# Performance work log

Hardware: AMD Instinct MI355X
Metric: run time of the kernel (lower is better)

## Reference

```python
import jax, jax.numpy as jnp
import numpy as np

K = 2  # top-k experts per token


def setup_inputs() -> dict:
    key = jax.random.key(0)
    k1, k2, k3, k4 = jax.random.split(key, 4)
    B, S, D, E = 4, 4096, 1024, 64
    x = jax.random.normal(k1, (B, S, D), dtype=jnp.float32)
    gate_w = jax.random.normal(k2, (E, D), dtype=jnp.float32) * (1.0 / np.sqrt(D))
    noise_weight = jax.random.normal(k3, (E,), dtype=jnp.float32) * 0.02
    noise = jax.random.normal(k4, (B, S, E), dtype=jnp.float32)  # randn_like(logits) * noisy_std(=1.0)
    return {"x": x, "gate_w": gate_w, "noise_weight": noise_weight, "noise": noise}


def reference(x, gate_w, noise_weight, noise):
    E = gate_w.shape[0]
    # logits = x @ W^T  -> [B, S, E]
    logits = jnp.einsum("bsd,ed->bse", x, gate_w)
    logits_noisy = logits + noise * noise_weight  # noisy_std = 1.0 folded into `noise`
    top_vals, top_idx = jax.lax.top_k(logits_noisy, K)  # [B,S,K]
    # scatter top-k logits into a -inf mask, then softmax over experts
    keep = jax.nn.one_hot(top_idx, E, dtype=jnp.bool_).any(axis=-2)  # [B,S,E]
    neg_inf = jnp.finfo(logits_noisy.dtype).min
    sparse = jnp.where(keep, logits_noisy, neg_inf)
    weights = jax.nn.softmax(sparse, axis=-1)
    return weights, top_idx
```

## Files before the change

### kernel.cpp

```cpp
#include <hip/hip_runtime.h>
#include <math.h>


#define DDIM 1024
#define NEXP 64
#define NTOK 16384

typedef float f4 __attribute__((ext_vector_type(4)));
typedef short s8 __attribute__((ext_vector_type(8)));
typedef unsigned int u32;

static __device__ __forceinline__ void split3(float f, short& h, short& m, short& l) {
    const u32 uf = __float_as_uint(f);
    h = (short)(uf >> 16);
    const float r1 = f - __uint_as_float(uf & 0xffff0000u);
    const u32 u1 = __float_as_uint(r1);
    m = (short)(u1 >> 16);
    const float r2 = r1 - __uint_as_float(u1 & 0xffff0000u);
    l = (short)(__float_as_uint(r2) >> 16);
}

__global__ __launch_bounds__(256)
void w_prep(const float* __restrict__ gw, short* __restrict__ wimg) {
    const int uid = blockIdx.x * 256 + threadIdx.x;
    const int c   = uid >> 9;
    const int kk  = (uid >> 8) & 1;
    const int e   = (uid >> 2) & 63;
    const int q   = uid & 3;
    const int k0  = c * 64 + kk * 32 + q * 8;
    const float* src = gw + (size_t)e * DDIM + k0;
    s8 hv, mv, lv;
    #pragma unroll
    for (int j = 0; j < 8; ++j) {
        short h, m, l;
        split3(src[j], h, m, l);
        hv[j] = h; mv[j] = m; lv[j] = l;
    }
    const size_t base = (size_t)c * 1536 + (kk * 3) * 256
                      + (e >> 4) * 64 + q * 16 + (e & 15);
    *(s8*)(wimg + (base      ) * 8) = hv;
    *(s8*)(wimg + (base + 256) * 8) = mv;
    *(s8*)(wimg + (base + 512) * 8) = lv;
}

__global__ __launch_bounds__(256, 4)
void gate_fused(const float* __restrict__ x,
                const short* __restrict__ wimg,
                const float* __restrict__ noise_weight,
                const float* __restrict__ noise,
                float* __restrict__ out_w,
                float* __restrict__ out_i)
{
    __shared__ float L[16][66];

    const int tid  = threadIdx.x;
    const int lane = tid & 63;
    const int wv   = tid >> 6;
    const int m    = lane & 15;
    const int q    = lane >> 4;
    const int tokBase = blockIdx.x * 16;

    const float* xrow = x + (size_t)(tokBase + m) * DDIM + q * 8;
    const short* wb   = wimg + ((size_t)wv * 64 + lane) * 8;

    const float nw = noise_weight[lane];
    float nz[4];
    #pragma unroll
    for (int tt = 0; tt < 4; ++tt)
        nz[tt] = noise[(size_t)(tokBase + wv * 4 + tt) * NEXP + lane];

    f4 acc0 = (f4)0.f, acc1 = (f4)0.f;

    f4 sa[2][4];
    s8 b[2][6];

    sa[0][0] = *(const f4*)(xrow);
    sa[0][1] = *(const f4*)(xrow + 4);
    sa[0][2] = *(const f4*)(xrow + 32);
    sa[0][3] = *(const f4*)(xrow + 36);
    #pragma unroll
    for (int i = 0; i < 6; ++i)
        b[0][i] = *(const s8*)(wb + (size_t)i * (256 * 8));

    #pragma unroll 2
    for (int cc = 0; cc < 16; ++cc) {
        const int cur = cc & 1;
        const int nxt = cur ^ 1;

        if (cc + 1 < 16) {
            const float* s = xrow + (cc + 1) * 64;
            sa[nxt][0] = *(const f4*)(s);
            sa[nxt][1] = *(const f4*)(s + 4);
            sa[nxt][2] = *(const f4*)(s + 32);
            sa[nxt][3] = *(const f4*)(s + 36);
            const short* p = wb + (size_t)(cc + 1) * (1536 * 8);
            #pragma unroll
            for (int i = 0; i < 6; ++i)
                b[nxt][i] = *(const s8*)(p + (size_t)i * (256 * 8));
        }

        s8 ah[2], am_[2], al[2];
        const float* sv = (const float*)sa[cur];
        #pragma unroll
        for (int kk = 0; kk < 2; ++kk)
            #pragma unroll
            for (int j = 0; j < 8; ++j) {
                short h, mm, l;
                split3(sv[kk * 8 + j], h, mm, l);
                ah[kk][j] = h; am_[kk][j] = mm; al[kk][j] = l;
            }

        acc0 = __builtin_amdgcn_mfma_f32_16x16x32_bf16(ah[0], b[cur][0], acc0, 0, 0, 0);
        acc1 = __builtin_amdgcn_mfma_f32_16x16x32_bf16(ah[0], b[cur][1], acc1, 0, 0, 0);
        acc1 = __builtin_amdgcn_mfma_f32_16x16x32_bf16(am_[0], b[cur][0], acc1, 0, 0, 0);
        acc1 = __builtin_amdgcn_mfma_f32_16x16x32_bf16(ah[0], b[cur][2], acc1, 0, 0, 0);
        acc1 = __builtin_amdgcn_mfma_f32_16x16x32_bf16(am_[0], b[cur][1], acc1, 0, 0, 0);
        acc1 = __builtin_amdgcn_mfma_f32_16x16x32_bf16(al[0], b[cur][0], acc1, 0, 0, 0);

        acc0 = __builtin_amdgcn_mfma_f32_16x16x32_bf16(ah[1], b[cur][3], acc0, 0, 0, 0);
        acc1 = __builtin_amdgcn_mfma_f32_16x16x32_bf16(ah[1], b[cur][4], acc1, 0, 0, 0);
        acc1 = __builtin_amdgcn_mfma_f32_16x16x32_bf16(am_[1], b[cur][3], acc1, 0, 0, 0);
        acc1 = __builtin_amdgcn_mfma_f32_16x16x32_bf16(ah[1], b[cur][5], acc1, 0, 0, 0);
        acc1 = __builtin_amdgcn_mfma_f32_16x16x32_bf16(am_[1], b[cur][4], acc1, 0, 0, 0);
        acc1 = __builtin_amdgcn_mfma_f32_16x16x32_bf16(al[1], b[cur][3], acc1, 0, 0, 0);
    }

    #pragma unroll
    for (int r = 0; r < 4; ++r)
        L[q * 4 + r][m + 16 * wv] = acc0[r] + acc1[r];
    __syncthreads();

    #pragma unroll
    for (int tt = 0; tt < 4; ++tt) {
        const int tok  = wv * 4 + tt;
        const int gtok = tokBase + tok;
        const float ln = fmaf(nz[tt], nw, L[tok][lane]);

        float v1 = ln; int i1 = lane;
        #pragma unroll
        for (int off = 32; off > 0; off >>= 1) {
            const float vo = __shfl_xor(v1, off, 64);
            const int   io = __shfl_xor(i1, off, 64);
            if (vo > v1 || (vo == v1 && io < i1)) { v1 = vo; i1 = io; }
        }
        float v2 = (lane == i1) ? -3.4e38f : ln; int i2 = lane;
        #pragma unroll
        for (int off = 32; off > 0; off >>= 1) {
            const float vo = __shfl_xor(v2, off, 64);
            const int   io = __shfl_xor(i2, off, 64);
            if (vo > v2 || (vo == v2 && io < i2)) { v2 = vo; i2 = io; }
        }

        const float d   = expf(v2 - v1);
        const float inv = 1.f / (1.f + d);
        const float wgt = (lane == i1) ? inv : ((lane == i2) ? d * inv : 0.f);
        out_w[(size_t)gtok * NEXP + lane] = wgt;
        if (lane == 0) {
            out_i[(size_t)gtok * 2]     = (float)i1;
            out_i[(size_t)gtok * 2 + 1] = (float)i2;
        }
    }
}

extern "C" void kernel_launch(void* const* d_in, const int* in_sizes, int n_in,
                              void* d_out, int out_size, void* d_ws, size_t ws_size,
                              hipStream_t stream) {
    const float* x     = (const float*)d_in[0];
    const float* gw    = (const float*)d_in[1];
    const float* nwt   = (const float*)d_in[2];
    const float* noise = (const float*)d_in[3];
    float* out_w = (float*)d_out;
    float* out_i = (float*)d_out + (size_t)NTOK * NEXP;

    short* wimg = (short*)d_ws;

    hipLaunchKernelGGL(w_prep, dim3(32), dim3(256), 0, stream, gw, wimg);
    hipLaunchKernelGGL(gate_fused, dim3(NTOK / 16), dim3(256), 0, stream,
                       x, wimg, nwt, noise, out_w, out_i);
}
```

Baseline: 146.2 us.

## Deepen software pipeline to two chunks ahead with sched barriers and perm-based bf16 packing

```diff
diff --git a/kernel.cpp b/kernel.cpp
--- a/kernel.cpp
+++ b/kernel.cpp
@@ -43,7 +43,57 @@
     *(s8*)(wimg + (base + 512) * 8) = lv;
 }
 
-__global__ __launch_bounds__(256, 4)
+static __device__ __forceinline__ u32 packhi(float flo, float fhi) {
+    return __builtin_amdgcn_perm(__float_as_uint(fhi), __float_as_uint(flo),
+                                 0x07060302u);
+}
+
+union FragU { u32 u[4]; s8 v; };
+
+static __device__ __forceinline__ void conv8(const float* f, s8& h, s8& m, s8& l) {
+    FragU H, M, L;
+    #pragma unroll
+    for (int j = 0; j < 4; ++j) {
+        const float f0 = f[2 * j], f1 = f[2 * j + 1];
+        H.u[j] = packhi(f0, f1);
+        const float g0 = f0 - __uint_as_float(__float_as_uint(f0) & 0xffff0000u);
+        const float g1 = f1 - __uint_as_float(__float_as_uint(f1) & 0xffff0000u);
+        M.u[j] = packhi(g0, g1);
+        const float e0 = g0 - __uint_as_float(__float_as_uint(g0) & 0xffff0000u);
+        const float e1 = g1 - __uint_as_float(__float_as_uint(g1) & 0xffff0000u);
+        L.u[j] = packhi(e0, e1);
+    }
+    h = H.v; m = M.v; l = L.v;
+}
+
+#define MF(A, B, C) __builtin_amdgcn_mfma_f32_16x16x32_bf16((A), (B), (C), 0, 0, 0)
+
+#define LOADA(S, P) { const float* _a = (P);                \
+    S[0] = *(const f4*)(_a);      S[1] = *(const f4*)(_a + 4);  \
+    S[2] = *(const f4*)(_a + 32); S[3] = *(const f4*)(_a + 36); }
+
+#define LOADB(B, P) { const short* _b = (P);                \
+    B[0] = *(const s8*)(_b);         B[1] = *(const s8*)(_b + 2048); \
+    B[2] = *(const s8*)(_b + 4096);  B[3] = *(const s8*)(_b + 6144); \
+    B[4] = *(const s8*)(_b + 8192);  B[5] = *(const s8*)(_b + 10240); }
+
+#define PART(SA, SB, NC)                                              \
+  {                                                                   \
+    s8 ah0, am0, al0, ah1, am1, al1;                                  \
+    conv8((const float*)&SA[0], ah0, am0, al0);                       \
+    conv8((const float*)&SA[2], ah1, am1, al1);                       \
+    if ((NC) < 16) LOADA(SA, xrow + (NC) * 64);                       \
+    acc0 = MF(ah0, SB[0], acc0);  acc1 = MF(ah0, SB[1], acc1);        \
+    acc1 = MF(am0, SB[0], acc1);  acc1 = MF(ah0, SB[2], acc1);        \
+    acc1 = MF(am0, SB[1], acc1);  acc1 = MF(al0, SB[0], acc1);        \
+    acc0 = MF(ah1, SB[3], acc0);  acc1 = MF(ah1, SB[4], acc1);        \
+    acc1 = MF(am1, SB[3], acc1);  acc1 = MF(ah1, SB[5], acc1);        \
+    acc1 = MF(am1, SB[4], acc1);  acc1 = MF(al1, SB[3], acc1);        \
+    if ((NC) < 16) LOADB(SB, wb + (size_t)(NC) * 12288);              \
+    __builtin_amdgcn_sched_barrier(0);                                \
+  }
+
+__global__ __launch_bounds__(256, 3)
 void gate_fused(const float* __restrict__ x,
                 const short* __restrict__ wimg,
                 const float* __restrict__ noise_weight,
@@ -51,7 +101,7 @@
                 float* __restrict__ out_w,
                 float* __restrict__ out_i)
 {
-    __shared__ float L[16][66];
+    __shared__ float Lds[16][66];
 
     const int tid  = threadIdx.x;
     const int lane = tid & 63;
@@ -71,70 +121,29 @@
 
     f4 acc0 = (f4)0.f, acc1 = (f4)0.f;
 
-    f4 sa[2][4];
-    s8 b[2][6];
+    f4 sa0[4], sa1[4];
+    s8 b0[6], b1[6];
 
-    sa[0][0] = *(const f4*)(xrow);
-    sa[0][1] = *(const f4*)(xrow + 4);
-    sa[0][2] = *(const f4*)(xrow + 32);
-    sa[0][3] = *(const f4*)(xrow + 36);
+    LOADA(sa0, xrow);           LOADB(b0, wb);
+    LOADA(sa1, xrow + 64);      LOADB(b1, wb + 12288);
+    __builtin_amdgcn_sched_barrier(0);
+
     #pragma unroll
-    for (int i = 0; i < 6; ++i)
-        b[0][i] = *(const s8*)(wb + (size_t)i * (256 * 8));
-
-    #pragma unroll 2
-    for (int cc = 0; cc < 16; ++cc) {
-        const int cur = cc & 1;
-        const int nxt = cur ^ 1;
-
-        if (cc + 1 < 16) {
-            const float* s = xrow + (cc + 1) * 64;
-            sa[nxt][0] = *(const f4*)(s);
-            sa[nxt][1] = *(const f4*)(s + 4);
-            sa[nxt][2] = *(const f4*)(s + 32);
-            sa[nxt][3] = *(const f4*)(s + 36);
-            const short* p = wb + (size_t)(cc + 1) * (1536 * 8);
-            #pragma unroll
-            for (int i = 0; i < 6; ++i)
-                b[nxt][i] = *(const s8*)(p + (size_t)i * (256 * 8));
-        }
-
-        s8 ah[2], am_[2], al[2];
-        const float* sv = (const float*)sa[cur];
-        #pragma unroll
-        for (int kk = 0; kk < 2; ++kk)
-            #pragma unroll
-            for (int j = 0; j < 8; ++j) {
-                short h, mm, l;
-                split3(sv[kk * 8 + j], h, mm, l);
-                ah[kk][j] = h; am_[kk][j] = mm; al[kk][j] = l;
-            }
-
-        acc0 = __builtin_amdgcn_mfma_f32_16x16x32_bf16(ah[0], b[cur][0], acc0, 0, 0, 0);
-        acc1 = __builtin_amdgcn_mfma_f32_16x16x32_bf16(ah[0], b[cur][1], acc1, 0, 0, 0);
-        acc1 = __builtin_amdgcn_mfma_f32_16x16x32_bf16(am_[0], b[cur][0], acc1, 0, 0, 0);
-        acc1 = __builtin_amdgcn_mfma_f32_16x16x32_bf16(ah[0], b[cur][2], acc1, 0, 0, 0);
-        acc1 = __builtin_amdgcn_mfma_f32_16x16x32_bf16(am_[0], b[cur][1], acc1, 0, 0, 0);
-        acc1 = __builtin_amdgcn_mfma_f32_16x16x32_bf16(al[0], b[cur][0], acc1, 0, 0, 0);
-
-        acc0 = __builtin_amdgcn_mfma_f32_16x16x32_bf16(ah[1], b[cur][3], acc0, 0, 0, 0);
-        acc1 = __builtin_amdgcn_mfma_f32_16x16x32_bf16(ah[1], b[cur][4], acc1, 0, 0, 0);
-        acc1 = __builtin_amdgcn_mfma_f32_16x16x32_bf16(am_[1], b[cur][3], acc1, 0, 0, 0);
-        acc1 = __builtin_amdgcn_mfma_f32_16x16x32_bf16(ah[1], b[cur][5], acc1, 0, 0, 0);
-        acc1 = __builtin_amdgcn_mfma_f32_16x16x32_bf16(am_[1], b[cur][4], acc1, 0, 0, 0);
-        acc1 = __builtin_amdgcn_mfma_f32_16x16x32_bf16(al[1], b[cur][3], acc1, 0, 0, 0);
+    for (int cc = 0; cc < 16; cc += 2) {
+        PART(sa0, b0, cc + 2);
+        PART(sa1, b1, cc + 3);
     }
 
     #pragma unroll
     for (int r = 0; r < 4; ++r)
-        L[q * 4 + r][m + 16 * wv] = acc0[r] + acc1[r];
+        Lds[q * 4 + r][m + 16 * wv] = acc0[r] + acc1[r];
     __syncthreads();
 
     #pragma unroll
     for (int tt = 0; tt < 4; ++tt) {
         const int tok  = wv * 4 + tt;
         const int gtok = tokBase + tok;
-        const float ln = fmaf(nz[tt], nw, L[tok][lane]);
+        const float ln = fmaf(nz[tt], nw, Lds[tok][lane]);
 
         float v1 = ln; int i1 = lane;
         #pragma unroll
```

Measured after the change: 144.5 us. About the same (-1.2%).
